# Optimization experiments

Measured on AMD Instinct MI355X. Metric: run time of the kernel, lower is better.

The kernel has to match this reference:

```python
import jax, jax.numpy as jnp
import numpy as np

D = 1024           # d_model
E = 8              # n_experts
H = 2752           # hidden = round_up64(round(1024 * 8/3))
N = 8192
ALPHA = 0.05       # load_balance_alpha
TEMP = 1.0         # router temperature


def setup_inputs() -> dict:
    key = jax.random.key(0)
    k0, k1, k2, k3, k4 = jax.random.split(key, 5)
    s_in = 1.0 / np.sqrt(D)   # kaiming-uniform-ish bound for Linear(in=D)
    s_h = 1.0 / np.sqrt(H)    # bound for down proj Linear(in=H)
    x = jax.random.normal(k0, (N, D), jnp.float32)
    Wg = jax.random.uniform(k1, (E, D), jnp.float32, -s_in, s_in)   # router weight [E, D]
    bg = jnp.zeros((E,), jnp.float32)                               # router bias
    Wu = jax.random.uniform(k2, (E, H, D), jnp.float32, -s_in, s_in)  # up_u weights (torch [out,in])
    Wv = jax.random.uniform(k3, (E, H, D), jnp.float32, -s_in, s_in)  # up_v weights
    Wd = jax.random.uniform(k4, (E, D, H), jnp.float32, -s_h, s_h)    # down weights
    return {"x": x, "Wg": Wg, "bg": bg, "Wu": Wu, "Wv": Wv, "Wd": Wd}


def reference(x, Wg, bg, Wu, Wv, Wd):
    # ---- Top-1 router (eval mode: no noise, temperature=1) ----
    logits = x @ Wg.T + bg                 # [N, E]
    logits_base = logits / TEMP
    probs = jax.nn.softmax(logits_base, axis=-1)
    top1_idx = jnp.argmax(logits_base, axis=-1)                          # [N]
    top1_p = jnp.take_along_axis(probs, top1_idx[:, None], axis=-1)[:, 0]  # [N]

    # Load-balance aux loss (both factors are no-grad in the torch code)
    me = jax.lax.stop_gradient(jnp.mean(jax.nn.one_hot(top1_idx, E, dtype=probs.dtype), axis=0))
    ce = jax.lax.stop_gradient(jnp.mean(probs, axis=0))
    aux = ALPHA * E * jnp.sum(me * ce)

    # ---- Dropless dispatch + per-expert SwiGLU + weighted combine ----
    # Loop over the small, fixed expert set; each token contributes only via
    # its selected expert (gate is zero elsewhere), matching masked dispatch.
    y = jnp.zeros_like(x)
    for e in range(E):
        u = x @ Wu[e].T                    # [N, H]
        v = x @ Wv[e].T                    # [N, H]
        ye = (jax.nn.silu(u) * v) @ Wd[e].T  # [N, D]
        gate = jnp.where(top1_idx == e, top1_p, 0.0)  # [N]
        y = y + ye * gate[:, None]
    return y, aux
```

## Files before the change

### kernel.cpp

```cpp
#include <hip/hip_runtime.h>
#include <hip/hip_bf16.h>

#define NTOK 8192
#define DMODEL 1024
#define NEXP 8
#define HID 2752
#define ALPHA 0.05f

#define BM 128
#define BN 128
#define BK 64
#define MAXTILES 72

typedef __attribute__((ext_vector_type(8))) short bf16x8;
typedef __attribute__((ext_vector_type(8))) unsigned short u16x8;
typedef __attribute__((ext_vector_type(4))) unsigned short u16x4;
typedef __attribute__((ext_vector_type(4))) float f32x4;

__device__ __forceinline__ unsigned short f2bf(float f){
  unsigned u = __builtin_bit_cast(unsigned, f);
  u += 0x7fffu + ((u >> 16) & 1u);
  return (unsigned short)(u >> 16);
}

__device__ __forceinline__ void gload16(const void* g, void* l){
  __builtin_amdgcn_global_load_lds(
      (const __attribute__((address_space(1))) unsigned int*)g,
      (__attribute__((address_space(3))) unsigned int*)l, 16, 0, 0);
}

__global__ void k_init(int* counts, int* cursor, float* ce_sum){
  int t = threadIdx.x;
  if (t < NEXP){ counts[t] = 0; cursor[t] = 0; ce_sum[t] = 0.f; }
}

__global__ __launch_bounds__(256) void k_pre(
    const float* __restrict__ Wu, const float* __restrict__ Wv, const float* __restrict__ Wd,
    unsigned short* __restrict__ Wub, unsigned short* __restrict__ Wvb,
    unsigned short* __restrict__ Wdb, int w8,
    const float* __restrict__ x, const float* __restrict__ Wg,
    const float* __restrict__ bg, int* __restrict__ counts,
    float* __restrict__ ce_sum, int* __restrict__ top1, float* __restrict__ gate,
    unsigned short* __restrict__ xb)
{
  __shared__ float wg[NEXP*DMODEL];
  __shared__ float ce_blk[NEXP];
  __shared__ int   cnt_blk[NEXP];
  const int tid = threadIdx.x;

  if ((int)blockIdx.x < 2048){
    const int tot = 3*w8;
    for (size_t i = (size_t)blockIdx.x*256 + tid; i < (size_t)tot; i += (size_t)2048*256){
      const float* s; unsigned short* d; size_t j;
      if (i < (size_t)w8)        { s = Wu; d = Wub; j = i; }
      else if (i < (size_t)2*w8) { s = Wv; d = Wvb; j = i - w8; }
      else                       { s = Wd; d = Wdb; j = i - 2*(size_t)w8; }
      const float4 a = ((const float4*)s)[j*2];
      const float4 b = ((const float4*)s)[j*2+1];
      u16x8 o;
      o[0]=f2bf(a.x); o[1]=f2bf(a.y); o[2]=f2bf(a.z); o[3]=f2bf(a.w);
      o[4]=f2bf(b.x); o[5]=f2bf(b.y); o[6]=f2bf(b.z); o[7]=f2bf(b.w);
      ((u16x8*)d)[j] = o;
    }
    return;
  }

  for (int i = tid; i < NEXP*DMODEL; i += 256) wg[i] = Wg[i];
  if (tid < NEXP){ ce_blk[tid] = 0.f; cnt_blk[tid] = 0; }
  __syncthreads();
  const int wave = tid >> 6, lane = tid & 63;
  const int t = ((int)blockIdx.x - 2048) * 4 + wave;
  float acc[NEXP];
  #pragma unroll
  for (int e = 0; e < NEXP; e++) acc[e] = 0.f;
  const float* xr = x + (size_t)t * DMODEL;
  unsigned short* xbr = xb + (size_t)t * DMODEL;
  #pragma unroll
  for (int kb = 0; kb < DMODEL; kb += 256){
    const float4 xv = *(const float4*)(xr + kb + lane*4);
    u16x4 o; o[0]=f2bf(xv.x); o[1]=f2bf(xv.y); o[2]=f2bf(xv.z); o[3]=f2bf(xv.w);
    *(u16x4*)(xbr + kb + lane*4) = o;
    #pragma unroll
    for (int e = 0; e < NEXP; e++){
      const float4 wv = *(const float4*)(wg + e*DMODEL + kb + lane*4);
      acc[e] += xv.x*wv.x + xv.y*wv.y + xv.z*wv.z + xv.w*wv.w;
    }
  }
  #pragma unroll
  for (int e = 0; e < NEXP; e++){
    float v = acc[e];
    #pragma unroll
    for (int off = 32; off; off >>= 1) v += __shfl_xor(v, off);
    acc[e] = v;
  }
  if (lane == 0){
    float mx = -1e30f; int bi = 0;
    float lg[NEXP];
    #pragma unroll
    for (int e = 0; e < NEXP; e++){
      lg[e] = acc[e] + bg[e];
      if (lg[e] > mx){ mx = lg[e]; bi = e; }
    }
    float s = 0.f, p[NEXP];
    #pragma unroll
    for (int e = 0; e < NEXP; e++){ p[e] = __expf(lg[e]-mx); s += p[e]; }
    const float inv = 1.f/s;
    #pragma unroll
    for (int e = 0; e < NEXP; e++) atomicAdd(&ce_blk[e], p[e]*inv);
    top1[t] = bi;
    gate[t] = p[bi]*inv;
    atomicAdd(&cnt_blk[bi], 1);
  }
  __syncthreads();
  if (tid < NEXP){
    atomicAdd(&counts[tid], cnt_blk[tid]);
    atomicAdd(&ce_sum[tid], ce_blk[tid]);
  }
}

__global__ void k_scan(const int* __restrict__ counts, const float* __restrict__ ce_sum,
                       int* offsets, int* nTiles, int* tileE, int* tileBase, int* tileCnt,
                       float* aux_out)
{
  if (threadIdx.x == 0){
    int off = 0;
    for (int e = 0; e < NEXP; e++){ offsets[e] = off; off += counts[e]; }
    offsets[NEXP] = off;
    int nt = 0;
    for (int e = 0; e < NEXP; e++){
      for (int r = 0; r < counts[e]; r += BM){
        tileE[nt] = e;
        tileBase[nt] = offsets[e] + r;
        int rem = counts[e] - r;
        tileCnt[nt] = rem < BM ? rem : BM;
        nt++;
      }
    }
    *nTiles = nt;
    float aux = 0.f;
    for (int e = 0; e < NEXP; e++)
      aux += ((float)counts[e] / (float)NTOK) * (ce_sum[e] / (float)NTOK);
    aux_out[0] = ALPHA * (float)NEXP * aux;
  }
}

__global__ __launch_bounds__(256) void k_scatter(const int* __restrict__ top1,
                                                 int* cursor, const int* __restrict__ offsets,
                                                 int* __restrict__ perm)
{
  const int t = blockIdx.x*256 + threadIdx.x;
  const int e = top1[t];
  const int lane = threadIdx.x & 63;
  int slot = 0;
  #pragma unroll
  for (int ee = 0; ee < NEXP; ee++){
    unsigned long long mask = __ballot(e == ee);
    if (e == ee){
      int leader = __ffsll(mask) - 1;
      int nbelow = __popcll(mask & ((1ull << lane) - 1ull));
      int base = 0;
      if (lane == leader) base = atomicAdd(&cursor[ee], __popcll(mask));
      base = __shfl(base, leader);
      slot = offsets[ee] + base + nbelow;
    }
  }
  perm[slot] = t;
}


__global__ __launch_bounds__(256,2) void k_up16(
    const unsigned short* __restrict__ xb,
    const unsigned short* __restrict__ Wub, const unsigned short* __restrict__ Wvb,
    const int* __restrict__ perm,
    const int* __restrict__ nTiles, const int* __restrict__ tileE,
    const int* __restrict__ tileBase, const int* __restrict__ tileCnt,
    unsigned short* __restrict__ h)
{
  const int l     = ((int)blockIdx.x % 8) * 198 + (int)blockIdx.x / 8;
  const int tileI = l % 72;
  const int ncol0 = (l / 72) * BN;
  if (tileI >= *nTiles) return;
  const int e    = tileE[tileI];
  const int base = tileBase[tileI];
  const int cnt  = tileCnt[tileI];

  __shared__ __align__(16) unsigned short As [BM*BK];
  __shared__ __align__(16) unsigned short Bus[BN*BK];
  __shared__ __align__(16) unsigned short Bvs[BN*BK];

  const int tid = threadIdx.x;
  const int wv = tid >> 6, ln = tid & 63;

  const unsigned short* srcA[4];
  const unsigned short* srcU[4];
  const unsigned short* srcV[4];
  #pragma unroll
  for (int c = 0; c < 4; c++){
    const int r  = wv*32 + c*8 + (ln>>3);
    const int sp = (ln&7) ^ (r&7);
    const int ra = (r < cnt) ? r : (cnt-1);
    srcA[c] = xb + (size_t)perm[base + ra]*DMODEL + sp*8;
    int rb = ncol0 + r; if (rb >= HID) rb = HID-1;
    srcU[c] = Wub + ((size_t)e*HID + rb)*DMODEL + sp*8;
    srcV[c] = Wvb + ((size_t)e*HID + rb)*DMODEL + sp*8;
  }

  const int wm = (wv >> 1) * 64, wn = (wv & 1) * 64;
  const int fr = ln & 15, fq = ln >> 4;

  f32x4 accU[4][4], accV[4][4];
  #pragma unroll
  for (int m = 0; m < 4; m++)
    #pragma unroll
    for (int n = 0; n < 4; n++)
      #pragma unroll
      for (int j = 0; j < 4; j++){ accU[m][n][j] = 0.f; accV[m][n][j] = 0.f; }

  for (int kb = 0; kb < DMODEL; kb += BK){
    #pragma unroll
    for (int c = 0; c < 4; c++){
      const unsigned ldo = wv*4096 + c*1024;
      gload16(srcA[c] + kb, (char*)As  + ldo);
      gload16(srcU[c] + kb, (char*)Bus + ldo);
      gload16(srcV[c] + kb, (char*)Bvs + ldo);
    }
    __syncthreads();
    #pragma unroll
    for (int ks = 0; ks < 2; ks++){
      bf16x8 af[4], bu[4], bv[4];
      #pragma unroll
      for (int m = 0; m < 4; m++){
        int r = wm + m*16 + fr;
        af[m] = *(const bf16x8*)((const char*)As + r*128 + ((ks*64 + fq*16) ^ ((r&7)<<4)));
      }
      #pragma unroll
      for (int n = 0; n < 4; n++){
        int r = wn + n*16 + fr;
        bu[n] = *(const bf16x8*)((const char*)Bus + r*128 + ((ks*64 + fq*16) ^ ((r&7)<<4)));
        bv[n] = *(const bf16x8*)((const char*)Bvs + r*128 + ((ks*64 + fq*16) ^ ((r&7)<<4)));
      }
      #pragma unroll
      for (int m = 0; m < 4; m++)
        #pragma unroll
        for (int n = 0; n < 4; n++){
          accU[m][n] = __builtin_amdgcn_mfma_f32_16x16x32_bf16(af[m], bu[n], accU[m][n], 0,0,0);
          accV[m][n] = __builtin_amdgcn_mfma_f32_16x16x32_bf16(af[m], bv[n], accV[m][n], 0,0,0);
        }
    }
    __syncthreads();
  }
  #pragma unroll
  for (int m = 0; m < 4; m++)
    #pragma unroll
    for (int n = 0; n < 4; n++)
      #pragma unroll
      for (int j = 0; j < 4; j++){
        int r = wm + m*16 + fq*4 + j;
        int c = ncol0 + wn + n*16 + fr;
        if (r < cnt && c < HID){
          float u = accU[m][n][j], v = accV[m][n][j];
          float hv = (u / (1.f + __expf(-u))) * v;
          h[(size_t)(base + r)*HID + c] = f2bf(hv);
        }
      }
}

__global__ __launch_bounds__(256,2) void k_down16(
    const unsigned short* __restrict__ h, const unsigned short* __restrict__ Wdb,
    const int* __restrict__ perm, const float* __restrict__ gate,
    const int* __restrict__ nTiles, const int* __restrict__ tileE,
    const int* __restrict__ tileBase, const int* __restrict__ tileCnt,
    float* __restrict__ out)
{
  const int l     = ((int)blockIdx.x % 8) * 72 + (int)blockIdx.x / 8;
  const int tileI = l % 72;
  const int ncol0 = (l / 72) * BN;
  if (tileI >= *nTiles) return;
  const int e    = tileE[tileI];
  const int base = tileBase[tileI];
  const int cnt  = tileCnt[tileI];

  __shared__ __align__(16) unsigned short As[BM*BK];
  __shared__ __align__(16) unsigned short Bs[BM*BK];
  __shared__ int   tokL[BM];
  __shared__ float gateL[BM];

  const int tid = threadIdx.x;
  if (tid < BM){
    int rr = (tid < cnt) ? tid : 0;
    int tk = perm[base + rr];
    tokL[tid] = tk;
    gateL[tid] = gate[tk];
  }
  const int wv = tid >> 6, ln = tid & 63;

  const unsigned short* srcA[4];
  const unsigned short* srcB[4];
  #pragma unroll
  for (int c = 0; c < 4; c++){
    const int r  = wv*32 + c*8 + (ln>>3);
    const int sp = (ln&7) ^ (r&7);
    const int ra = (r < cnt) ? r : (cnt-1);
    srcA[c] = h + (size_t)(base + ra)*HID + sp*8;
    const int rb = ncol0 + r;
    srcB[c] = Wdb + ((size_t)e*DMODEL + rb)*HID + sp*8;
  }

  const int wm = (wv >> 1) * 64, wn = (wv & 1) * 64;
  const int fr = ln & 15, fq = ln >> 4;

  f32x4 acc[4][4];
  #pragma unroll
  for (int m = 0; m < 4; m++)
    #pragma unroll
    for (int n = 0; n < 4; n++)
      #pragma unroll
      for (int j = 0; j < 4; j++) acc[m][n][j] = 0.f;

  for (int kb = 0; kb < HID; kb += BK){
    #pragma unroll
    for (int c = 0; c < 4; c++){
      const unsigned ldo = wv*4096 + c*1024;
      gload16(srcA[c] + kb, (char*)As + ldo);
      gload16(srcB[c] + kb, (char*)Bs + ldo);
    }
    __syncthreads();
    #pragma unroll
    for (int ks = 0; ks < 2; ks++){
      bf16x8 af[4], bf[4];
      #pragma unroll
      for (int m = 0; m < 4; m++){
        int r = wm + m*16 + fr;
        af[m] = *(const bf16x8*)((const char*)As + r*128 + ((ks*64 + fq*16) ^ ((r&7)<<4)));
      }
      #pragma unroll
      for (int n = 0; n < 4; n++){
        int r = wn + n*16 + fr;
        bf[n] = *(const bf16x8*)((const char*)Bs + r*128 + ((ks*64 + fq*16) ^ ((r&7)<<4)));
      }
      #pragma unroll
      for (int m = 0; m < 4; m++)
        #pragma unroll
        for (int n = 0; n < 4; n++)
          acc[m][n] = __builtin_amdgcn_mfma_f32_16x16x32_bf16(af[m], bf[n], acc[m][n], 0,0,0);
    }
    __syncthreads();
  }
  #pragma unroll
  for (int m = 0; m < 4; m++)
    #pragma unroll
    for (int n = 0; n < 4; n++)
      #pragma unroll
      for (int j = 0; j < 4; j++){
        int r = wm + m*16 + fq*4 + j;
        int c = ncol0 + wn + n*16 + fr;
        if (r < cnt)
          out[(size_t)tokL[r]*DMODEL + c] = acc[m][n][j] * gateL[r];
      }
}

extern "C" void kernel_launch(void* const* d_in, const int* in_sizes, int n_in,
                              void* d_out, int out_size, void* d_ws, size_t ws_size,
                              hipStream_t stream)
{
  const float* x  = (const float*)d_in[0];
  const float* Wg = (const float*)d_in[1];
  const float* bg = (const float*)d_in[2];
  const float* Wu = (const float*)d_in[3];
  const float* Wv = (const float*)d_in[4];
  const float* Wd = (const float*)d_in[5];
  float* out = (float*)d_out;

  char* ws = (char*)d_ws;
  int*   counts   = (int*)(ws + 0);
  int*   cursor   = (int*)(ws + 32);
  int*   offsets  = (int*)(ws + 64);
  float* ce_sum   = (float*)(ws + 128);
  int*   nTiles   = (int*)(ws + 192);
  int*   tileE    = (int*)(ws + 256);
  int*   tileBase = (int*)(ws + 768);
  int*   tileCnt  = (int*)(ws + 1280);
  int*   top1     = (int*)(ws + 2048);
  float* gate     = (float*)(ws + 34816);
  int*   perm     = (int*)(ws + 67584);
  unsigned short* xb   = (unsigned short*)(ws + 100352);
  unsigned short* hbuf = (unsigned short*)(ws + 100352 + (size_t)NTOK*DMODEL*2);
  const size_t W_ELEMS = (size_t)NEXP*HID*DMODEL;
  const size_t baseW = 100352 + (size_t)NTOK*DMODEL*2 + (size_t)NTOK*HID*2;
  unsigned short* Wub = (unsigned short*)(ws + baseW);
  unsigned short* Wvb = (unsigned short*)(ws + baseW + W_ELEMS*2);
  unsigned short* Wdb = (unsigned short*)(ws + baseW + W_ELEMS*4);

  k_init<<<1, 64, 0, stream>>>(counts, cursor, ce_sum);
  k_pre<<<4096, 256, 0, stream>>>(Wu, Wv, Wd, Wub, Wvb, Wdb, (int)(W_ELEMS/8),
                                  x, Wg, bg, counts, ce_sum, top1, gate, xb);
  k_scan<<<1, 64, 0, stream>>>(counts, ce_sum, offsets, nTiles, tileE, tileBase, tileCnt,
                               out + (size_t)NTOK*DMODEL);
  k_scatter<<<NTOK/256, 256, 0, stream>>>(top1, cursor, offsets, perm);

  k_up16<<<MAXTILES*((HID + BN - 1)/BN), 256, 0, stream>>>(
      xb, Wub, Wvb, perm, nTiles, tileE, tileBase, tileCnt, hbuf);
  k_down16<<<MAXTILES*(DMODEL/BN), 256, 0, stream>>>(
      hbuf, Wdb, perm, gate, nTiles, tileE, tileBase, tileCnt, out);
}
```

Measured before the change: 348.5 us.

## Split fused up-projection into separate U and V GEMM kernels

The fused dual-accumulator up-projection kernel is split into two kernels. The first computes x·Wu and stores u as bf16 into the h buffer. The second computes x·Wv, reads u back, applies SiLU(u)·v and overwrites h. This halves accumulator registers and LDS per block so launch bounds can rise to 3 blocks per SM, including for the down kernel. The cost is an extra read and write of the N×H intermediate, reloading the x tiles a second time, and rounding u to bf16 before SiLU.

```diff
diff --git a/kernel.cpp b/kernel.cpp
--- a/kernel.cpp
+++ b/kernel.cpp
@@ -21,6 +21,9 @@
   unsigned u = __builtin_bit_cast(unsigned, f);
   u += 0x7fffu + ((u >> 16) & 1u);
   return (unsigned short)(u >> 16);
+}
+__device__ __forceinline__ float bf2f(unsigned short s){
+  return __builtin_bit_cast(float, ((unsigned)s) << 16);
 }
 
 __device__ __forceinline__ void gload16(const void* g, void* l){
@@ -168,9 +171,8 @@
 }
 
 
-__global__ __launch_bounds__(256,2) void k_up16(
-    const unsigned short* __restrict__ xb,
-    const unsigned short* __restrict__ Wub, const unsigned short* __restrict__ Wvb,
+__global__ __launch_bounds__(256,3) void k_upU(
+    const unsigned short* __restrict__ xb, const unsigned short* __restrict__ Wub,
     const int* __restrict__ perm,
     const int* __restrict__ nTiles, const int* __restrict__ tileE,
     const int* __restrict__ tileBase, const int* __restrict__ tileCnt,
@@ -184,16 +186,14 @@
   const int base = tileBase[tileI];
   const int cnt  = tileCnt[tileI];
 
-  __shared__ __align__(16) unsigned short As [BM*BK];
-  __shared__ __align__(16) unsigned short Bus[BN*BK];
-  __shared__ __align__(16) unsigned short Bvs[BN*BK];
+  __shared__ __align__(16) unsigned short As[BM*BK];
+  __shared__ __align__(16) unsigned short Bs[BN*BK];
 
   const int tid = threadIdx.x;
   const int wv = tid >> 6, ln = tid & 63;
 
   const unsigned short* srcA[4];
-  const unsigned short* srcU[4];
-  const unsigned short* srcV[4];
+  const unsigned short* srcB[4];
   #pragma unroll
   for (int c = 0; c < 4; c++){
     const int r  = wv*32 + c*8 + (ln>>3);
@@ -201,33 +201,31 @@
     const int ra = (r < cnt) ? r : (cnt-1);
     srcA[c] = xb + (size_t)perm[base + ra]*DMODEL + sp*8;
     int rb = ncol0 + r; if (rb >= HID) rb = HID-1;
-    srcU[c] = Wub + ((size_t)e*HID + rb)*DMODEL + sp*8;
-    srcV[c] = Wvb + ((size_t)e*HID + rb)*DMODEL + sp*8;
+    srcB[c] = Wub + ((size_t)e*HID + rb)*DMODEL + sp*8;
   }
 
   const int wm = (wv >> 1) * 64, wn = (wv & 1) * 64;
   const int fr = ln & 15, fq = ln >> 4;
 
-  f32x4 accU[4][4], accV[4][4];
-  #pragma unroll
-  for (int m = 0; m < 4; m++)
-    #pragma unroll
-    for (int n = 0; n < 4; n++)
-      #pragma unroll
-      for (int j = 0; j < 4; j++){ accU[m][n][j] = 0.f; accV[m][n][j] = 0.f; }
+  f32x4 acc[4][4];
+  #pragma unroll
+  for (int m = 0; m < 4; m++)
+    #pragma unroll
+    for (int n = 0; n < 4; n++)
+      #pragma unroll
+      for (int j = 0; j < 4; j++) acc[m][n][j] = 0.f;
 
   for (int kb = 0; kb < DMODEL; kb += BK){
     #pragma unroll
     for (int c = 0; c < 4; c++){
       const unsigned ldo = wv*4096 + c*1024;
-      gload16(srcA[c] + kb, (char*)As  + ldo);
-      gload16(srcU[c] + kb, (char*)Bus + ldo);
-      gload16(srcV[c] + kb, (char*)Bvs + ldo);
+      gload16(srcA[c] + kb, (char*)As + ldo);
+      gload16(srcB[c] + kb, (char*)Bs + ldo);
     }
     __syncthreads();
     #pragma unroll
     for (int ks = 0; ks < 2; ks++){
-      bf16x8 af[4], bu[4], bv[4];
+      bf16x8 af[4], bf[4];
       #pragma unroll
       for (int m = 0; m < 4; m++){
         int r = wm + m*16 + fr;
@@ -236,16 +234,99 @@
       #pragma unroll
       for (int n = 0; n < 4; n++){
         int r = wn + n*16 + fr;
-        bu[n] = *(const bf16x8*)((const char*)Bus + r*128 + ((ks*64 + fq*16) ^ ((r&7)<<4)));
-        bv[n] = *(const bf16x8*)((const char*)Bvs + r*128 + ((ks*64 + fq*16) ^ ((r&7)<<4)));
+        bf[n] = *(const bf16x8*)((const char*)Bs + r*128 + ((ks*64 + fq*16) ^ ((r&7)<<4)));
       }
       #pragma unroll
       for (int m = 0; m < 4; m++)
         #pragma unroll
-        for (int n = 0; n < 4; n++){
-          accU[m][n] = __builtin_amdgcn_mfma_f32_16x16x32_bf16(af[m], bu[n], accU[m][n], 0,0,0);
-          accV[m][n] = __builtin_amdgcn_mfma_f32_16x16x32_bf16(af[m], bv[n], accV[m][n], 0,0,0);
-        }
+        for (int n = 0; n < 4; n++)
+          acc[m][n] = __builtin_amdgcn_mfma_f32_16x16x32_bf16(af[m], bf[n], acc[m][n], 0,0,0);
+    }
+    __syncthreads();
+  }
+  #pragma unroll
+  for (int m = 0; m < 4; m++)
+    #pragma unroll
+    for (int n = 0; n < 4; n++)
+      #pragma unroll
+      for (int j = 0; j < 4; j++){
+        int r = wm + m*16 + fq*4 + j;
+        int c = ncol0 + wn + n*16 + fr;
+        if (r < cnt && c < HID)
+          h[(size_t)(base + r)*HID + c] = f2bf(acc[m][n][j]);
+      }
+}
+
+__global__ __launch_bounds__(256,3) void k_upV(
+    const unsigned short* __restrict__ xb, const unsigned short* __restrict__ Wvb,
+    const int* __restrict__ perm,
+    const int* __restrict__ nTiles, const int* __restrict__ tileE,
+    const int* __restrict__ tileBase, const int* __restrict__ tileCnt,
+    unsigned short* __restrict__ h)
+{
+  const int l     = ((int)blockIdx.x % 8) * 198 + (int)blockIdx.x / 8;
+  const int tileI = l % 72;
+  const int ncol0 = (l / 72) * BN;
+  if (tileI >= *nTiles) return;
+  const int e    = tileE[tileI];
+  const int base = tileBase[tileI];
+  const int cnt  = tileCnt[tileI];
+
+  __shared__ __align__(16) unsigned short As[BM*BK];
+  __shared__ __align__(16) unsigned short Bs[BN*BK];
+
+  const int tid = threadIdx.x;
+  const int wv = tid >> 6, ln = tid & 63;
+
+  const unsigned short* srcA[4];
+  const unsigned short* srcB[4];
+  #pragma unroll
+  for (int c = 0; c < 4; c++){
+    const int r  = wv*32 + c*8 + (ln>>3);
+    const int sp = (ln&7) ^ (r&7);
+    const int ra = (r < cnt) ? r : (cnt-1);
+    srcA[c] = xb + (size_t)perm[base + ra]*DMODEL + sp*8;
+    int rb = ncol0 + r; if (rb >= HID) rb = HID-1;
+    srcB[c] = Wvb + ((size_t)e*HID + rb)*DMODEL + sp*8;
+  }
+
+  const int wm = (wv >> 1) * 64, wn = (wv & 1) * 64;
+  const int fr = ln & 15, fq = ln >> 4;
+
+  f32x4 acc[4][4];
+  #pragma unroll
+  for (int m = 0; m < 4; m++)
+    #pragma unroll
+    for (int n = 0; n < 4; n++)
+      #pragma unroll
+      for (int j = 0; j < 4; j++) acc[m][n][j] = 0.f;
+
+  for (int kb = 0; kb < DMODEL; kb += BK){
+    #pragma unroll
+    for (int c = 0; c < 4; c++){
+      const unsigned ldo = wv*4096 + c*1024;
+      gload16(srcA[c] + kb, (char*)As + ldo);
+      gload16(srcB[c] + kb, (char*)Bs + ldo);
+    }
+    __syncthreads();
+    #pragma unroll
+    for (int ks = 0; ks < 2; ks++){
+      bf16x8 af[4], bf[4];
+      #pragma unroll
+      for (int m = 0; m < 4; m++){
+        int r = wm + m*16 + fr;
+        af[m] = *(const bf16x8*)((const char*)As + r*128 + ((ks*64 + fq*16) ^ ((r&7)<<4)));
+      }
+      #pragma unroll
+      for (int n = 0; n < 4; n++){
+        int r = wn + n*16 + fr;
+        bf[n] = *(const bf16x8*)((const char*)Bs + r*128 + ((ks*64 + fq*16) ^ ((r&7)<<4)));
+      }
+      #pragma unroll
+      for (int m = 0; m < 4; m++)
+        #pragma unroll
+        for (int n = 0; n < 4; n++)
+          acc[m][n] = __builtin_amdgcn_mfma_f32_16x16x32_bf16(af[m], bf[n], acc[m][n], 0,0,0);
     }
     __syncthreads();
   }
@@ -258,14 +339,15 @@
         int r = wm + m*16 + fq*4 + j;
         int c = ncol0 + wn + n*16 + fr;
         if (r < cnt && c < HID){
-          float u = accU[m][n][j], v = accV[m][n][j];
-          float hv = (u / (1.f + __expf(-u))) * v;
-          h[(size_t)(base + r)*HID + c] = f2bf(hv);
+          const size_t idx = (size_t)(base + r)*HID + c;
+          float u = bf2f(h[idx]);
+          float hv = (u / (1.f + __expf(-u))) * acc[m][n][j];
+          h[idx] = f2bf(hv);
         }
       }
 }
 
-__global__ __launch_bounds__(256,2) void k_down16(
+__global__ __launch_bounds__(256,3) void k_down16(
     const unsigned short* __restrict__ h, const unsigned short* __restrict__ Wdb,
     const int* __restrict__ perm, const float* __restrict__ gate,
     const int* __restrict__ nTiles, const int* __restrict__ tileE,
@@ -398,8 +480,9 @@
                                out + (size_t)NTOK*DMODEL);
   k_scatter<<<NTOK/256, 256, 0, stream>>>(top1, cursor, offsets, perm);
 
-  k_up16<<<MAXTILES*((HID + BN - 1)/BN), 256, 0, stream>>>(
-      xb, Wub, Wvb, perm, nTiles, tileE, tileBase, tileCnt, hbuf);
+  const int gUp = MAXTILES*((HID + BN - 1)/BN);
+  k_upU<<<gUp, 256, 0, stream>>>(xb, Wub, perm, nTiles, tileE, tileBase, tileCnt, hbuf);
+  k_upV<<<gUp, 256, 0, stream>>>(xb, Wvb, perm, nTiles, tileE, tileBase, tileCnt, hbuf);
   k_down16<<<MAXTILES*(DMODEL/BN), 256, 0, stream>>>(
       hbuf, Wdb, perm, gate, nTiles, tileE, tileBase, tileCnt, out);
 }
```

Result: slower. 405.1 us (+16.2%).
